# Kernel optimization log

Hardware: AMD Instinct MI355X
Metric: run time of the kernel (lower is better)

The kernel has to match this reference:

```python
import jax, jax.numpy as jnp
import numpy as np

N = 50000      # nodes
E = 800000     # edges (avg degree 16)
F_IN = 128     # num_features
HID = 128      # hidden_channels
C = 40         # num_classes


def setup_inputs() -> dict:
    key = jax.random.key(0)
    ks = jax.random.split(key, 8)
    x = jax.random.normal(ks[0], (N, F_IN), dtype=jnp.float32)
    edge_index = jax.random.randint(ks[1], (2, E), 0, N, dtype=jnp.int64)
    def glorot(k, fan_in, fan_out):
        s = np.sqrt(6.0 / (fan_in + fan_out)).astype(np.float32)
        return jax.random.uniform(k, (fan_in, fan_out), jnp.float32, -s, s)
    return {
        "x": x,
        "W1": glorot(ks[2], F_IN, HID), "b1": jnp.zeros((HID,), jnp.float32),
        "W2": glorot(ks[3], HID, HID),  "b2": jnp.zeros((HID,), jnp.float32),
        "W3": glorot(ks[4], HID, C),   "b3": jnp.zeros((C,), jnp.float32),
        "edge_index": edge_index,
    }


def reference(x, W1, b1, W2, b2, W3, b3, edge_index):
    # GCN with symmetric normalization and self-loops (PyG GCNConv semantics),
    # eval mode (dropout p=0.0), log-softmax output.
    src = edge_index[0]
    dst = edge_index[1]
    loop = jnp.arange(N, dtype=edge_index.dtype)
    src = jnp.concatenate([src, loop])      # [E+N]
    dst = jnp.concatenate([dst, loop])      # [E+N]
    ew = jnp.ones((E + N,), jnp.float32)    # edge_weight=None -> ones
    # deg[i] = sum of incoming edge weights at node i (aggregation index = dst/col)
    deg = jax.ops.segment_sum(ew, dst, num_segments=N)
    dinv = jnp.where(deg > 0, jax.lax.rsqrt(deg), 0.0)
    norm = dinv[src] * ew * dinv[dst]       # [E+N]

    def conv(h, W, b):
        # linear transform first (no bias), then gather->scale->scatter-add, then bias
        m = (h @ W)[src] * norm[:, None]                      # [E+N, out]
        return jax.ops.segment_sum(m, dst, num_segments=N) + b

    h = jax.nn.relu(conv(x, W1, b1))
    h = jax.nn.relu(conv(h, W2, b2))
    h = conv(h, W3, b3)
    return jax.nn.log_softmax(h, axis=-1)
```

## Files before the change

kernel.cpp:

```cpp
#include <hip/hip_runtime.h>
#include <math.h>

#define N_NODES 50000
#define N_EDGES 800000
#define BUCKET 64
#define SCAT_BLKS 196
#define GEMM_BLKS 196

typedef __attribute__((ext_vector_type(8))) short short8;
typedef __attribute__((ext_vector_type(4))) float f32x4;

__device__ __forceinline__ ushort f2bf(float f) {
    union { float f; uint u; } v; v.f = f;
    uint r = v.u + 0x7FFFu + ((v.u >> 16) & 1u);
    return (ushort)(r >> 16);
}
__device__ __forceinline__ float bflo(uint p) {
    union { uint u; float f; } v; v.u = p << 16; return v.f;
}
__device__ __forceinline__ float bfhi(uint p) {
    union { uint u; float f; } v; v.u = p & 0xFFFF0000u; return v.f;
}

__global__ __launch_bounds__(512) void fused_gemm1_scatter_k(
        const float* __restrict__ Af, const float* __restrict__ W, ushort* __restrict__ Y,
        const int* __restrict__ src, const int* __restrict__ dst,
        int* __restrict__ cnt, ushort* __restrict__ colb) {
    constexpr int NT = 8;
    __shared__ ushort sB[4 * NT * 64 * 8];
    const int tid = threadIdx.x;

    if (blockIdx.x < SCAT_BLKS) {
        const int t = blockIdx.x * 512 + tid;
        if (t >= N_EDGES / 8) return;
        const int4* s32 = reinterpret_cast<const int4*>(src);
        const int4* d32 = reinterpret_cast<const int4*>(dst);
        const int4 sa = s32[2 * t], sb = s32[2 * t + 1];
        const int4 da = d32[2 * t], db = d32[2 * t + 1];
        int p0 = atomicAdd(&cnt[da.x], 1);
        int p1 = atomicAdd(&cnt[da.y], 1);
        int p2 = atomicAdd(&cnt[da.z], 1);
        int p3 = atomicAdd(&cnt[da.w], 1);
        int p4 = atomicAdd(&cnt[db.x], 1);
        int p5 = atomicAdd(&cnt[db.y], 1);
        int p6 = atomicAdd(&cnt[db.z], 1);
        int p7 = atomicAdd(&cnt[db.w], 1);
        colb[(size_t)da.x * BUCKET + p0] = (ushort)sa.x;
        colb[(size_t)da.y * BUCKET + p1] = (ushort)sa.y;
        colb[(size_t)da.z * BUCKET + p2] = (ushort)sa.z;
        colb[(size_t)da.w * BUCKET + p3] = (ushort)sa.w;
        colb[(size_t)db.x * BUCKET + p4] = (ushort)sb.x;
        colb[(size_t)db.y * BUCKET + p5] = (ushort)sb.y;
        colb[(size_t)db.z * BUCKET + p6] = (ushort)sb.z;
        colb[(size_t)db.w * BUCKET + p7] = (ushort)sb.w;
        return;
    }

    constexpr int FP = NT * 16;
    for (int i = tid; i < 128 * FP; i += 512) {
        const int k = i / FP, n = i % FP;
        const int s = k >> 5, r2 = (k >> 3) & 3, j = k & 7;
        const int t = n >> 4, nl = n & 15;
        const int l = r2 * 16 + nl;
        const int lp = (l & 56) | ((l + (l >> 3)) & 7);
        sB[(((s * NT + t) * 64) + lp) * 8 + j] = f2bf(W[k * 128 + n]);
    }
    __syncthreads();

    const int wid = tid >> 6, lane = tid & 63;
    const int lp = (lane & 56) | ((lane + (lane >> 3)) & 7);
    const int t0 = (blockIdx.x - SCAT_BLKS) * 16 + wid * 2;
    const int t1 = t0 + 1;
    const int t0c = min(t0, N_NODES / 16 - 1);
    const int t1c = min(t1, N_NODES / 16 - 1);

    f32x4 acc[2][NT];
#pragma unroll
    for (int u = 0; u < 2; u++)
#pragma unroll
        for (int t = 0; t < NT; t++) acc[u][t] = (f32x4){0.f, 0.f, 0.f, 0.f};

#pragma unroll
    for (int s = 0; s < 4; s++) {
        short8 a0, a1;
        const int ko = 32 * s + 8 * (lane >> 4);
        const float4* p0 = reinterpret_cast<const float4*>(Af + (size_t)(t0c * 16 + (lane & 15)) * 128 + ko);
        const float4* p1 = reinterpret_cast<const float4*>(Af + (size_t)(t1c * 16 + (lane & 15)) * 128 + ko);
        float4 u0 = p0[0], u1 = p0[1], v0 = p1[0], v1 = p1[1];
        a0[0] = f2bf(u0.x); a0[1] = f2bf(u0.y); a0[2] = f2bf(u0.z); a0[3] = f2bf(u0.w);
        a0[4] = f2bf(u1.x); a0[5] = f2bf(u1.y); a0[6] = f2bf(u1.z); a0[7] = f2bf(u1.w);
        a1[0] = f2bf(v0.x); a1[1] = f2bf(v0.y); a1[2] = f2bf(v0.z); a1[3] = f2bf(v0.w);
        a1[4] = f2bf(v1.x); a1[5] = f2bf(v1.y); a1[6] = f2bf(v1.z); a1[7] = f2bf(v1.w);
#pragma unroll
        for (int t = 0; t < NT; t++) {
            short8 b = *reinterpret_cast<const short8*>(&sB[(((s * NT + t) * 64) + lp) * 8]);
            acc[0][t] = __builtin_amdgcn_mfma_f32_16x16x32_bf16(a0, b, acc[0][t], 0, 0, 0);
            acc[1][t] = __builtin_amdgcn_mfma_f32_16x16x32_bf16(a1, b, acc[1][t], 0, 0, 0);
        }
    }

    const int rl = 4 * (lane >> 4), cl = lane & 15;
#pragma unroll
    for (int u = 0; u < 2; u++) {
        const int tile = u ? t1 : t0;
        if (tile >= N_NODES / 16) continue;
        const int row0 = tile * 16;
#pragma unroll
        for (int t = 0; t < NT; t++) {
            const int c = 16 * t + cl;
#pragma unroll
            for (int g = 0; g < 4; g++)
                Y[(size_t)(row0 + rl + g) * 128 + c] = f2bf(acc[u][t][g]);
        }
    }
}

template <int NT>
__global__ __launch_bounds__(512) void gemm_scaled_k(const ushort* __restrict__ Ab,
                                                     const float* __restrict__ W,
                                                     const int* __restrict__ cnt,
                                                     ushort* __restrict__ Y,
                                                     const int fout) {
    __shared__ ushort sB[4 * NT * 64 * 8];
    const int tid = threadIdx.x;
    constexpr int FP = NT * 16;
    for (int i = tid; i < 128 * FP; i += 512) {
        const int k = i / FP, n = i % FP;
        const int s = k >> 5, r2 = (k >> 3) & 3, j = k & 7;
        const int t = n >> 4, nl = n & 15;
        const int l = r2 * 16 + nl;
        const int lp = (l & 56) | ((l + (l >> 3)) & 7);
        sB[(((s * NT + t) * 64) + lp) * 8 + j] = (n < fout) ? f2bf(W[k * fout + n]) : (ushort)0;
    }
    __syncthreads();

    const int wid = tid >> 6, lane = tid & 63;
    const int lp = (lane & 56) | ((lane + (lane >> 3)) & 7);
    const int t0 = blockIdx.x * 16 + wid * 2;
    const int t1 = t0 + 1;
    const int t0c = min(t0, N_NODES / 16 - 1);
    const int t1c = min(t1, N_NODES / 16 - 1);

    f32x4 acc[2][NT];
#pragma unroll
    for (int u = 0; u < 2; u++)
#pragma unroll
        for (int t = 0; t < NT; t++) acc[u][t] = (f32x4){0.f, 0.f, 0.f, 0.f};

#pragma unroll
    for (int s = 0; s < 4; s++) {
        const int ko = 32 * s + 8 * (lane >> 4);
        short8 a0 = *reinterpret_cast<const short8*>(Ab + (size_t)(t0c * 16 + (lane & 15)) * 128 + ko);
        short8 a1 = *reinterpret_cast<const short8*>(Ab + (size_t)(t1c * 16 + (lane & 15)) * 128 + ko);
#pragma unroll
        for (int t = 0; t < NT; t++) {
            short8 b = *reinterpret_cast<const short8*>(&sB[(((s * NT + t) * 64) + lp) * 8]);
            acc[0][t] = __builtin_amdgcn_mfma_f32_16x16x32_bf16(a0, b, acc[0][t], 0, 0, 0);
            acc[1][t] = __builtin_amdgcn_mfma_f32_16x16x32_bf16(a1, b, acc[1][t], 0, 0, 0);
        }
    }

    const int rl = 4 * (lane >> 4), cl = lane & 15;
#pragma unroll
    for (int u = 0; u < 2; u++) {
        const int tile = u ? t1 : t0;
        if (tile >= N_NODES / 16) continue;
        const int row0 = tile * 16;
#pragma unroll
        for (int g = 0; g < 4; g++) {
            const int row = row0 + rl + g;
            const float dr = rsqrtf((float)(cnt[row] + 1));
#pragma unroll
            for (int t = 0; t < NT; t++) {
                const int c = 16 * t + cl;
                if (NT == 3 && c >= fout) continue;
                Y[(size_t)row * fout + c] = f2bf(acc[u][t][g] * dr);
            }
        }
    }
}

__global__ __launch_bounds__(256) void gather1_k(const ushort* __restrict__ XW,
                                                 const int* __restrict__ cnt,
                                                 const ushort* __restrict__ colb,
                                                 const float* __restrict__ bias,
                                                 ushort* __restrict__ out) {
    const int node = (blockIdx.x * 256 + threadIdx.x) >> 6;
    const int lane = threadIdx.x & 63;
    if (node >= N_NODES) return;
    const int n = cnt[node];
    const float di = rsqrtf((float)(n + 1));
    int sl = 0; float wl = 0.f;
    if (lane < n) {
        sl = colb[(size_t)node * BUCKET + lane];
        wl = rsqrtf((float)(cnt[sl] + 1));
    }
    const uint* XW32 = reinterpret_cast<const uint*>(XW);

    float a0 = 0.f, a1 = 0.f, b0 = 0.f, b1 = 0.f;
    float c0 = 0.f, c1 = 0.f, d0 = 0.f, d1 = 0.f;
    int e = 0;
    for (; e + 4 <= n; e += 4) {
        const int s0 = __shfl(sl, e),     s1 = __shfl(sl, e + 1);
        const int s2 = __shfl(sl, e + 2), s3 = __shfl(sl, e + 3);
        const float w0 = __shfl(wl, e),     w1 = __shfl(wl, e + 1);
        const float w2 = __shfl(wl, e + 2), w3 = __shfl(wl, e + 3);
        const uint p0 = XW32[(size_t)s0 * 64 + lane];
        const uint p1 = XW32[(size_t)s1 * 64 + lane];
        const uint p2 = XW32[(size_t)s2 * 64 + lane];
        const uint p3 = XW32[(size_t)s3 * 64 + lane];
        a0 = fmaf(bflo(p0), w0, a0); a1 = fmaf(bfhi(p0), w0, a1);
        b0 = fmaf(bflo(p1), w1, b0); b1 = fmaf(bfhi(p1), w1, b1);
        c0 = fmaf(bflo(p2), w2, c0); c1 = fmaf(bfhi(p2), w2, c1);
        d0 = fmaf(bflo(p3), w3, d0); d1 = fmaf(bfhi(p3), w3, d1);
    }
    for (; e < n; e++) {
        const int s = __shfl(sl, e);
        const float w = __shfl(wl, e);
        const uint p = XW32[(size_t)s * 64 + lane];
        a0 = fmaf(bflo(p), w, a0); a1 = fmaf(bfhi(p), w, a1);
    }
    const uint ps = XW32[(size_t)node * 64 + lane];
    float t0 = (a0 + b0) + (c0 + d0); t0 = fmaf(bflo(ps), di, t0);
    float t1 = (a1 + b1) + (c1 + d1); t1 = fmaf(bfhi(ps), di, t1);
    const float o0 = fmaxf(fmaf(di, t0, bias[2 * lane]), 0.f);
    const float o1 = fmaxf(fmaf(di, t1, bias[2 * lane + 1]), 0.f);
    reinterpret_cast<uint*>(out)[(size_t)node * 64 + lane] =
        (uint)f2bf(o0) | ((uint)f2bf(o1) << 16);
}

__global__ __launch_bounds__(256) void gather_add_k(const ushort* __restrict__ XWn,
                                                    const int* __restrict__ cnt,
                                                    const ushort* __restrict__ colb,
                                                    const float* __restrict__ bias,
                                                    ushort* __restrict__ out) {
    const int node = (blockIdx.x * 256 + threadIdx.x) >> 6;
    const int lane = threadIdx.x & 63;
    if (node >= N_NODES) return;
    const int n = cnt[node];
    const float di = rsqrtf((float)(n + 1));
    const ushort4* bucket = reinterpret_cast<const ushort4*>(colb + (size_t)node * BUCKET);
    const uint* XW32 = reinterpret_cast<const uint*>(XWn);

    float a0 = 0.f, a1 = 0.f, b0 = 0.f, b1 = 0.f;
    float c0 = 0.f, c1 = 0.f, d0 = 0.f, d1 = 0.f;
    int e = 0;
    for (; e + 4 <= n; e += 4) {
        const ushort4 s4 = bucket[e >> 2];
        const uint p0 = XW32[(size_t)s4.x * 64 + lane];
        const uint p1 = XW32[(size_t)s4.y * 64 + lane];
        const uint p2 = XW32[(size_t)s4.z * 64 + lane];
        const uint p3 = XW32[(size_t)s4.w * 64 + lane];
        a0 += bflo(p0); a1 += bfhi(p0);
        b0 += bflo(p1); b1 += bfhi(p1);
        c0 += bflo(p2); c1 += bfhi(p2);
        d0 += bflo(p3); d1 += bfhi(p3);
    }
    for (; e < n; e++) {
        const ushort s = colb[(size_t)node * BUCKET + e];
        const uint p = XW32[(size_t)s * 64 + lane];
        a0 += bflo(p); a1 += bfhi(p);
    }
    const uint ps = XW32[(size_t)node * 64 + lane];
    const float t0 = ((a0 + b0) + (c0 + d0)) + bflo(ps);
    const float t1 = ((a1 + b1) + (c1 + d1)) + bfhi(ps);
    const float o0 = fmaxf(fmaf(di, t0, bias[2 * lane]), 0.f);
    const float o1 = fmaxf(fmaf(di, t1, bias[2 * lane + 1]), 0.f);
    reinterpret_cast<uint*>(out)[(size_t)node * 64 + lane] =
        (uint)f2bf(o0) | ((uint)f2bf(o1) << 16);
}

__global__ __launch_bounds__(256) void gather40_lsm_k(const ushort* __restrict__ XWn,
                                                      const int* __restrict__ cnt,
                                                      const ushort* __restrict__ colb,
                                                      const float* __restrict__ bias,
                                                      float* __restrict__ out) {
    const int node = (blockIdx.x * 256 + threadIdx.x) >> 6;
    const int lane = threadIdx.x & 63;
    if (node >= N_NODES) return;
    const int g = lane < 20 ? 0 : (lane < 40 ? 1 : 2);
    const int ll = lane - g * 20;
    const int llc = min(ll, 19);
    const int n = cnt[node];
    const float di = rsqrtf((float)(n + 1));
    const uint* XW32 = reinterpret_cast<const uint*>(XWn);

    float a0 = 0.f, a1 = 0.f;
    for (int e = g; e < n; e += 3) {
        const ushort s = colb[(size_t)node * BUCKET + e];
        const uint p = XW32[(size_t)s * 20 + llc];
        a0 += bflo(p); a1 += bfhi(p);
    }
    const float t1 = __shfl(a0, lane + 20), t2 = __shfl(a0, lane + 40);
    const float u1 = __shfl(a1, lane + 20), u2 = __shfl(a1, lane + 40);
    float v0 = -INFINITY, v1 = -INFINITY;
    if (lane < 20) {
        const uint ps = XW32[(size_t)node * 20 + lane];
        v0 = fmaf(di, (a0 + t1 + t2) + bflo(ps), bias[2 * lane]);
        v1 = fmaf(di, (a1 + u1 + u2) + bfhi(ps), bias[2 * lane + 1]);
    }
    float m = fmaxf(v0, v1);
#pragma unroll
    for (int o = 32; o > 0; o >>= 1) m = fmaxf(m, __shfl_xor(m, o));
    float s = (lane < 20) ? (expf(v0 - m) + expf(v1 - m)) : 0.f;
#pragma unroll
    for (int o = 32; o > 0; o >>= 1) s += __shfl_xor(s, o);
    if (lane < 20) {
        const float ls = m + logf(s);
        float2 r; r.x = v0 - ls; r.y = v1 - ls;
        reinterpret_cast<float2*>(out)[(size_t)node * 20 + lane] = r;
    }
}

extern "C" void kernel_launch(void* const* d_in, const int* in_sizes, int n_in,
                              void* d_out, int out_size, void* d_ws, size_t ws_size,
                              hipStream_t stream) {
    const float* x  = (const float*)d_in[0];
    const float* W1 = (const float*)d_in[1];
    const float* b1 = (const float*)d_in[2];
    const float* W2 = (const float*)d_in[3];
    const float* b2 = (const float*)d_in[4];
    const float* W3 = (const float*)d_in[5];
    const float* b3 = (const float*)d_in[6];
    const int* ei   = (const int*)d_in[7];
    const int* srcp = ei;
    const int* dstp = ei + N_EDGES;
    float* out = (float*)d_out;

    int*    cnt  = (int*)d_ws;
    ushort* colb = (ushort*)(cnt + 50176);
    ushort* B0   = colb + (size_t)N_NODES * BUCKET;
    ushort* B1   = B0 + (size_t)N_NODES * 128;

    const int NB_W = (N_NODES * 64) / 256;

    hipMemsetAsync(cnt, 0, 50176 * sizeof(int), stream);
    fused_gemm1_scatter_k<<<SCAT_BLKS + GEMM_BLKS, 512, 0, stream>>>(
        x, W1, B1, srcp, dstp, cnt, colb);
    gather1_k<<<NB_W, 256, 0, stream>>>(B1, cnt, colb, b1, B0);
    gemm_scaled_k<8><<<GEMM_BLKS, 512, 0, stream>>>(B0, W2, cnt, B1, 128);
    gather_add_k<<<NB_W, 256, 0, stream>>>(B1, cnt, colb, b2, B0);
    gemm_scaled_k<3><<<GEMM_BLKS, 512, 0, stream>>>(B0, W3, cnt, B1, 40);
    gather40_lsm_k<<<NB_W, 256, 0, stream>>>(B1, cnt, colb, b3, out);
}
```

Measured before the change: 270.3 us.

## Partition edge bucketing by destination range across blocks for atomic locality

The scatter phase is restructured so each scatter block handles one of 8 destination-node ranges of 6250 nodes. Each block scans a slice of edges and processes only edges whose destination falls in its range. The aim is to confine atomics and bucket writes to a smaller address window per block, improving cache/L2 locality of the cnt and colb updates (on MI355X, blocks with r = blockIdx & 7 may also map to the same XCD). In exchange, every edge's dst is read 8 times and the scatter block count doubles, adding memory traffic and divergent branches.

```diff
diff --git a/kernel.cpp b/kernel.cpp
--- a/kernel.cpp
+++ b/kernel.cpp
@@ -4,7 +4,8 @@
 #define N_NODES 50000
 #define N_EDGES 800000
 #define BUCKET 64
-#define SCAT_BLKS 196
+#define SCAT_BLKS 392
+#define QPG 4082
 #define GEMM_BLKS 196
 
 typedef __attribute__((ext_vector_type(8))) short short8;
@@ -31,28 +32,37 @@
     const int tid = threadIdx.x;
 
     if (blockIdx.x < SCAT_BLKS) {
-        const int t = blockIdx.x * 512 + tid;
-        if (t >= N_EDGES / 8) return;
+        const int r = blockIdx.x & 7;
+        const int g = blockIdx.x >> 3;
+        const int lo = r * 6250;
         const int4* s32 = reinterpret_cast<const int4*>(src);
         const int4* d32 = reinterpret_cast<const int4*>(dst);
-        const int4 sa = s32[2 * t], sb = s32[2 * t + 1];
-        const int4 da = d32[2 * t], db = d32[2 * t + 1];
-        int p0 = atomicAdd(&cnt[da.x], 1);
-        int p1 = atomicAdd(&cnt[da.y], 1);
-        int p2 = atomicAdd(&cnt[da.z], 1);
-        int p3 = atomicAdd(&cnt[da.w], 1);
-        int p4 = atomicAdd(&cnt[db.x], 1);
-        int p5 = atomicAdd(&cnt[db.y], 1);
-        int p6 = atomicAdd(&cnt[db.z], 1);
-        int p7 = atomicAdd(&cnt[db.w], 1);
-        colb[(size_t)da.x * BUCKET + p0] = (ushort)sa.x;
-        colb[(size_t)da.y * BUCKET + p1] = (ushort)sa.y;
-        colb[(size_t)da.z * BUCKET + p2] = (ushort)sa.z;
-        colb[(size_t)da.w * BUCKET + p3] = (ushort)sa.w;
-        colb[(size_t)db.x * BUCKET + p4] = (ushort)sb.x;
-        colb[(size_t)db.y * BUCKET + p5] = (ushort)sb.y;
-        colb[(size_t)db.z * BUCKET + p6] = (ushort)sb.z;
-        colb[(size_t)db.w * BUCKET + p7] = (ushort)sb.w;
+        const int qbeg = g * QPG + tid;
+        const int qend = min((g + 1) * QPG, N_EDGES / 4);
+#pragma unroll
+        for (int u = 0; u < 8; u++) {
+            const int q = qbeg + u * 512;
+            if (q < qend) {
+                const int4 d4 = d32[q];
+                const int4 s4 = s32[q];
+                if ((uint)(d4.x - lo) < 6250u) {
+                    int p = atomicAdd(&cnt[d4.x], 1);
+                    colb[(size_t)d4.x * BUCKET + p] = (ushort)s4.x;
+                }
+                if ((uint)(d4.y - lo) < 6250u) {
+                    int p = atomicAdd(&cnt[d4.y], 1);
+                    colb[(size_t)d4.y * BUCKET + p] = (ushort)s4.y;
+                }
+                if ((uint)(d4.z - lo) < 6250u) {
+                    int p = atomicAdd(&cnt[d4.z], 1);
+                    colb[(size_t)d4.z * BUCKET + p] = (ushort)s4.z;
+                }
+                if ((uint)(d4.w - lo) < 6250u) {
+                    int p = atomicAdd(&cnt[d4.w], 1);
+                    colb[(size_t)d4.w * BUCKET + p] = (ushort)s4.w;
+                }
+            }
+        }
         return;
     }
 
```

Measured after the change: 263.3 us. 2.6% less time.
